# Kernel optimization log

Measured on AMD Instinct MI355X. Metric: run time of the kernel, lower is better.

## Reference

```python
import jax, jax.numpy as jnp
import numpy as np

B, D, DEPTH, H, E, N, NC = 128, 192, 12, 3, 4, 65, 100
WIN_HALF = 3  # window_size=7 -> |i-j| <= 3


def _ln(x, g, b, eps=1e-5):
    m = x.mean(-1, keepdims=True)
    v = ((x - m) ** 2).mean(-1, keepdims=True)
    return (x - m) / jnp.sqrt(v + eps) * g + b


def _forward(x, conv_w, conv_b, pe_g, pe_b, cls_token, pos_embed,
             n1_g, n1_b, qkv_w, temp, proj_w, proj_b, n2_g, n2_b,
             gate_w, gate_b, e_w1, e_b1, e_w2, e_b2, attn_scale, mlp_scale,
             norm_g, norm_b, hc_w, hc_b, head_w, head_b):
    Bx = x.shape[0]
    # patch embed: conv with kernel==stride==4 is a blocked matmul
    p = x.reshape(Bx, 3, 8, 4, 8, 4).transpose(0, 2, 4, 1, 3, 5).reshape(Bx, 64, 48)
    t = p @ conv_w.reshape(D, 48).T + conv_b
    t = _ln(t, pe_g, pe_b)
    t = jnp.concatenate([jnp.broadcast_to(cls_token, (Bx, 1, D)), t], axis=1) + pos_embed
    Nn = t.shape[1]
    hd = D // H
    scale = hd ** -0.5
    idx = jnp.arange(Nn)
    # local-window attention mask (log of {0,1} -> {-inf,0})
    mask = jnp.where(jnp.abs(idx[:, None] - idx[None, :]) <= WIN_HALF, 0.0, -jnp.inf)
    for l in range(DEPTH):
        # --- attention ---
        y = _ln(t, n1_g[l], n1_b[l])
        qkv = (y @ qkv_w[l].T).reshape(Bx, Nn, 3, H, hd).transpose(2, 0, 3, 1, 4)
        q, k, v = qkv[0], qkv[1], qkv[2]
        a = (q @ k.transpose(0, 1, 3, 2)) * scale / temp[l]  # [B,H,N,N]
        a = jax.nn.softmax(a + mask, axis=-1)
        o = (a @ v).transpose(0, 2, 1, 3).reshape(Bx, Nn, D)
        o = o @ proj_w[l].T + proj_b[l]
        t = t + attn_scale[l] * o
        # --- top-2 MoE (dense-equivalent of the masked per-expert dispatch) ---
        y = _ln(t, n2_g[l], n2_b[l])
        g = jax.nn.softmax(y @ gate_w[l].T + gate_b[l], axis=-1)  # [B,N,E]
        tg, ti = jax.lax.top_k(g, 2)
        tg = tg / tg.sum(-1, keepdims=True)
        h = jax.nn.gelu(jnp.einsum('bnc,ehc->bneh', y, e_w1[l]) + e_b1[l], approximate=False)
        eo = jnp.einsum('bneh,ech->bnec', h, e_w2[l]) + e_b2[l]  # [B,N,E,C]
        sel = jnp.take_along_axis(eo, ti[..., None], axis=2)  # [B,N,2,C]
        mo = (sel * tg[..., None]).sum(axis=2)
        t = t + mlp_scale[l] * mo
    t = _ln(t, norm_g, norm_b)
    cls = t[:, 0]
    # hypercomplex linear head: out[:,k] += x[:,j] @ W[(k-j)%n].T
    xv = cls.reshape(Bx, E, D // E)
    perm = (jnp.arange(E)[:, None] - jnp.arange(E)[None, :]) % E  # [k,j] -> i
    hh = jnp.einsum('bjc,kjoc->bko', xv, hc_w[perm]).reshape(Bx, 2 * D) + hc_b
    hh = jax.nn.gelu(hh, approximate=False)
    return hh @ head_w.T + head_b


def setup_inputs() -> dict:
    ks = iter(jax.random.split(jax.random.key(0), 64))
    def rn(shape, s=0.02):
        return jax.random.normal(next(ks), shape, jnp.float32) * s
    return dict(
        x=jax.random.normal(next(ks), (B, 3, 32, 32), jnp.float32),
        conv_w=rn((D, 3, 4, 4)), conv_b=jnp.zeros((D,)),
        pe_g=jnp.ones((D,)), pe_b=jnp.zeros((D,)),
        cls_token=rn((1, 1, D)), pos_embed=rn((1, N, D)),
        n1_g=jnp.ones((DEPTH, D)), n1_b=jnp.zeros((DEPTH, D)),
        qkv_w=rn((DEPTH, 3 * D, D)), temp=jnp.ones((DEPTH, H, 1, 1)),
        proj_w=rn((DEPTH, D, D)), proj_b=jnp.zeros((DEPTH, D)),
        n2_g=jnp.ones((DEPTH, D)), n2_b=jnp.zeros((DEPTH, D)),
        gate_w=rn((DEPTH, E, D)), gate_b=jnp.zeros((DEPTH, E)),
        e_w1=rn((DEPTH, E, 2 * D, D)), e_b1=jnp.zeros((DEPTH, E, 2 * D)),
        e_w2=rn((DEPTH, E, D, 2 * D)), e_b2=jnp.zeros((DEPTH, E, D)),
        attn_scale=jnp.ones((DEPTH,)), mlp_scale=jnp.ones((DEPTH,)),
        norm_g=jnp.ones((D,)), norm_b=jnp.zeros((D,)),
        hc_w=rn((E, 2 * D // E, D // E)), hc_b=jnp.zeros((2 * D,)),
        head_w=rn((NC, 2 * D)), head_b=jnp.zeros((NC,)),
    )


def reference(x, conv_w, conv_b, pe_g, pe_b, cls_token, pos_embed,
              n1_g, n1_b, qkv_w, temp, proj_w, proj_b, n2_g, n2_b,
              gate_w, gate_b, e_w1, e_b1, e_w2, e_b2, attn_scale, mlp_scale,
              norm_g, norm_b, hc_w, hc_b, head_w, head_b):
    return _forward(x, conv_w, conv_b, pe_g, pe_b, cls_token, pos_embed,
                    n1_g, n1_b, qkv_w, temp, proj_w, proj_b, n2_g, n2_b,
                    gate_w, gate_b, e_w1, e_b1, e_w2, e_b2, attn_scale, mlp_scale,
                    norm_g, norm_b, hc_w, hc_b, head_w, head_b)
```

## Files before the change

### kernel.cpp

```cpp
#include <hip/hip_runtime.h>
#include <cmath>

#define ROWS 8320
#define DD   192

typedef __attribute__((ext_vector_type(8))) _Float16 half8;
typedef __attribute__((ext_vector_type(4))) float floatx4;

#define GLD16(gp, lp) __builtin_amdgcn_global_load_lds( \
    (const __attribute__((address_space(1))) void*)(gp), \
    (__attribute__((address_space(3))) void*)(lp), 16, 0, 0)

#define MFMA_F16 __builtin_amdgcn_mfma_f32_16x16x32_f16

__device__ __forceinline__ float gelu_f(float x) {
    return 0.5f * x * (1.0f + erff(x * 0.70710678118654752440f));
}

__device__ __forceinline__ float blk_sum_192(float v, float* sbuf) {
    int tid = threadIdx.x;
    sbuf[tid] = v;
    __syncthreads();
    for (int off = 96; off >= 3; off >>= 1) {
        if (tid < off) sbuf[tid] += sbuf[tid + off];
        __syncthreads();
    }
    float r = sbuf[0] + sbuf[1] + sbuf[2];
    __syncthreads();
    return r;
}

__global__ __launch_bounds__(256) void cvt_h_kernel(
    const float* __restrict__ s, _Float16* __restrict__ d, long n8)
{
    long i = (long)blockIdx.x * 256 + threadIdx.x;
    if (i >= n8) return;
    const float* sp = s + i * 8;
    _Float16* dp = d + i * 8;
    #pragma unroll
    for (int j = 0; j < 8; j++) dp[j] = (_Float16)sp[j];
}

__global__ __launch_bounds__(256) void permw2h_kernel(
    const float* __restrict__ s, _Float16* __restrict__ d)
{
    long i = (long)blockIdx.x * 256 + threadIdx.x;
    if (i >= (long)12 * 192 * 192) return;
    int l = (int)(i / (192 * 192));
    int rem = (int)(i % (192 * 192));
    int n = rem / 192, p = rem % 192;
    int c0 = p * 8;
    int e = c0 / 384, k0 = c0 % 384;
    const float* sp = s + (((size_t)l * 4 + e) * 192 + n) * 384 + k0;
    _Float16* dp = d + i * 8;
    #pragma unroll
    for (int j = 0; j < 8; j++) dp[j] = (_Float16)sp[j];
}

__global__ __launch_bounds__(192) void embed_kernel(
    const float* __restrict__ x, const float* __restrict__ conv_w,
    const float* __restrict__ conv_b, const float* __restrict__ pe_g,
    const float* __restrict__ pe_b, const float* __restrict__ cls_tok,
    const float* __restrict__ pos, float* __restrict__ t)
{
    __shared__ float patch[48];
    __shared__ float red[192];
    int blk = blockIdx.x;
    int b = blk / 65, n = blk % 65;
    int tid = threadIdx.x;
    if (n == 0) {
        t[(size_t)b * 65 * DD + tid] = cls_tok[tid] + pos[tid];
        return;
    }
    int p = n - 1, gy = p / 8, gx = p % 8;
    if (tid < 48) {
        int c = tid / 16, iy = (tid % 16) / 4, ix = tid % 4;
        patch[tid] = x[((size_t)b * 3 + c) * 1024 + (size_t)(gy * 4 + iy) * 32 + (gx * 4 + ix)];
    }
    __syncthreads();
    float s = conv_b[tid];
    const float* w = conv_w + (size_t)tid * 48;
    #pragma unroll
    for (int f = 0; f < 48; f++) s += patch[f] * w[f];
    float mean = blk_sum_192(s, red) * (1.0f / 192.0f);
    float d = s - mean;
    float var = blk_sum_192(d * d, red) * (1.0f / 192.0f);
    float o = d * rsqrtf(var + 1e-5f) * pe_g[tid] + pe_b[tid];
    t[((size_t)b * 65 + n) * DD + tid] = o + pos[(size_t)n * DD + tid];
}

__global__ __launch_bounds__(256) void ln_kernel(
    const float* __restrict__ in, const float* __restrict__ ctb,
    float* __restrict__ tout,
    float* __restrict__ yf, _Float16* __restrict__ yh,
    const float* __restrict__ g, const float* __restrict__ bb, long in_stride, int nrows,
    const float* __restrict__ gwm, const float* __restrict__ gb,
    int4* __restrict__ gwout)
{
    int wave = threadIdx.x >> 6, lane = threadIdx.x & 63;
    int r = blockIdx.x * 4 + wave;
    if (r >= nrows) return;
    const float* row = in + (size_t)r * in_stride;
    float v0 = row[lane], v1 = row[lane + 64], v2 = row[lane + 128];
    if (ctb) {
        long gr = (long)r * (in_stride / DD);
        const float* cb = ctb + gr * 384;
        v0 += cb[lane] + cb[192 + lane];
        v1 += cb[lane + 64] + cb[256 + lane];
        v2 += cb[lane + 128] + cb[320 + lane];
        if (tout) {
            float* tr = tout + (size_t)r * in_stride;
            tr[lane] = v0; tr[lane + 64] = v1; tr[lane + 128] = v2;
        }
    }
    float s = v0 + v1 + v2;
    #pragma unroll
    for (int off = 32; off > 0; off >>= 1) s += __shfl_xor(s, off);
    float mean = s * (1.0f / 192.0f);
    float d0 = v0 - mean, d1 = v1 - mean, d2 = v2 - mean;
    float q = d0 * d0 + d1 * d1 + d2 * d2;
    #pragma unroll
    for (int off = 32; off > 0; off >>= 1) q += __shfl_xor(q, off);
    float rstd = rsqrtf(q * (1.0f / 192.0f) + 1e-5f);
    float o0 = d0 * rstd * g[lane] + bb[lane];
    float o1 = d1 * rstd * g[lane + 64] + bb[lane + 64];
    float o2 = d2 * rstd * g[lane + 128] + bb[lane + 128];
    if (yf) {
        float* yr = yf + (size_t)r * DD;
        yr[lane] = o0; yr[lane + 64] = o1; yr[lane + 128] = o2;
    }
    if (yh) {
        _Float16* yr = yh + (size_t)r * DD;
        yr[lane] = (_Float16)o0; yr[lane + 64] = (_Float16)o1; yr[lane + 128] = (_Float16)o2;
    }
    if (gwm) {
        float pe[4];
        #pragma unroll
        for (int e = 0; e < 4; e++) {
            const float* w = gwm + (size_t)e * DD;
            pe[e] = o0 * w[lane] + o1 * w[lane + 64] + o2 * w[lane + 128];
            #pragma unroll
            for (int off = 32; off > 0; off >>= 1) pe[e] += __shfl_xor(pe[e], off);
        }
        if (lane == 0) {
            #pragma unroll
            for (int e = 0; e < 4; e++) pe[e] += gb[e];
            float mx = fmaxf(fmaxf(pe[0], pe[1]), fmaxf(pe[2], pe[3]));
            float ex[4];
            #pragma unroll
            for (int e = 0; e < 4; e++) ex[e] = expf(pe[e] - mx);
            int i0 = 0;
            #pragma unroll
            for (int e = 1; e < 4; e++) if (ex[e] > ex[i0]) i0 = e;
            int i1 = (i0 == 0) ? 1 : 0;
            #pragma unroll
            for (int e = 0; e < 4; e++) if (e != i0 && ex[e] > ex[i1]) i1 = e;
            float denom = ex[i0] + ex[i1];
            int4 o4;
            o4.x = i0; o4.y = i1;
            o4.z = __float_as_int(ex[i0] / denom);
            o4.w = __float_as_int(ex[i1] / denom);
            gwout[r] = o4;
        }
    }
}

__global__ __launch_bounds__(256) void gate_build_kernel(
    const int4* __restrict__ gwrow, int* __restrict__ cnt,
    int* __restrict__ list, float* __restrict__ wlist, int rows)
{
    int r = blockIdx.x * 256 + threadIdx.x;
    int lane = threadIdx.x & 63;
    bool active = r < rows;
    int4 gv = active ? gwrow[r] : int4{-1, -1, 0, 0};
    #pragma unroll
    for (int e = 0; e < 4; e++) {
        bool sel = active && (gv.x == e || gv.y == e);
        int rank = (gv.x == e) ? 0 : 1;
        float w = (gv.x == e) ? __int_as_float(gv.z) : __int_as_float(gv.w);
        unsigned long long mask = __ballot(sel);
        int cw = __popcll(mask);
        if (cw) {
            int leader = __ffsll((long long)mask) - 1;
            int base = 0;
            if (lane == leader) base = atomicAdd(&cnt[e], cw);
            base = __shfl(base, leader);
            if (sel) {
                int idx = base + __popcll(mask & ((1ULL << lane) - 1ULL));
                list[(size_t)e * ROWS + idx] = (r << 1) | rank;
                wlist[(size_t)e * ROWS + idx] = w;
            }
        }
    }
}

template <int MODE>
__global__ __launch_bounds__(256) void gemm_h(
    const _Float16* __restrict__ A, const _Float16* __restrict__ W,
    int Nn, _Float16* __restrict__ outH, float* __restrict__ t,
    const float* __restrict__ bias, const float* __restrict__ scale)
{
    __shared__ __align__(16) _Float16 As[64 * 192];
    __shared__ __align__(16) _Float16 Ws[64 * 192];
    const int tid = threadIdx.x;
    const int lane = tid & 63, wave = tid >> 6;
    const int m0 = blockIdx.x * 64, n0 = blockIdx.y * 64;
    const int wm = (wave & 1) * 32, wn = (wave >> 1) * 32;
    const int lr = lane & 15, quad = lane >> 4;

    #pragma unroll
    for (int i = 0; i < 6; i++) {
        int s = (wave * 6 + i) * 64 + lane;
        int rr = s / 24, c = s % 24;
        GLD16(A + (size_t)(m0 + rr) * 192 + (c ^ (rr & 7)) * 8,
              (char*)As + (size_t)(wave * 6 + i) * 1024);
        GLD16(W + (size_t)(n0 + rr) * 192 + (c ^ (rr & 7)) * 8,
              (char*)Ws + (size_t)(wave * 6 + i) * 1024);
    }
    __syncthreads();

    floatx4 zero = {0.f, 0.f, 0.f, 0.f};
    floatx4 acc[2][2];
    acc[0][0] = zero; acc[0][1] = zero; acc[1][0] = zero; acc[1][1] = zero;

    #pragma unroll
    for (int m = 0; m < 6; m++) {
        int ch = m * 4 + quad;
        half8 a[2], w[2];
        #pragma unroll
        for (int ti = 0; ti < 2; ti++) {
            int ar = wm + ti * 16 + lr;
            a[ti] = *(const half8*)(As + ((size_t)ar * 24 + (ch ^ (ar & 7))) * 8);
            int cr = wn + ti * 16 + lr;
            w[ti] = *(const half8*)(Ws + ((size_t)cr * 24 + (ch ^ (cr & 7))) * 8);
        }
        #pragma unroll
        for (int ti = 0; ti < 2; ti++)
            #pragma unroll
            for (int tj = 0; tj < 2; tj++)
                acc[ti][tj] = MFMA_F16(a[ti], w[tj], acc[ti][tj], 0, 0, 0);
    }

    float sc = (MODE == 2) ? scale[0] : 0.f;
    #pragma unroll
    for (int ti = 0; ti < 2; ti++)
        #pragma unroll
        for (int tj = 0; tj < 2; tj++)
            #pragma unroll
            for (int r = 0; r < 4; r++) {
                int grow = m0 + wm + ti * 16 + quad * 4 + r;
                int gcol = n0 + wn + tj * 16 + lr;
                float v = acc[ti][tj][r];
                if (MODE == 0) {
                    float vp = __shfl_xor(v, 1);
                    if ((lane & 1) == 0) {
                        union { _Float16 h[2]; unsigned u; } pk;
                        pk.h[0] = (_Float16)v;
                        pk.h[1] = (_Float16)vp;
                        *(unsigned*)(outH + (size_t)grow * Nn + (gcol & ~1)) = pk.u;
                    }
                } else {
                    t[(size_t)grow * DD + gcol] += sc * (v + bias[gcol]);
                }
            }
}

__global__ __launch_bounds__(256) void moe_kernel(
    const _Float16* __restrict__ yh, const _Float16* __restrict__ w1,
    const _Float16* __restrict__ w2, const float* __restrict__ b1,
    const float* __restrict__ b2, const float* __restrict__ scale,
    const int* __restrict__ cnt, const int* __restrict__ list,
    const float* __restrict__ wlist, float* __restrict__ ctb)
{
    __shared__ __align__(16) _Float16 As[32 * 192];
    __shared__ __align__(16) _Float16 W1s[64 * 192];
    __shared__ __align__(16) _Float16 W2s[192 * 64];
    __shared__ __align__(16) _Float16 Hs[32 * 64];
    __shared__ int   rl[32];
    __shared__ int   rk[32];
    __shared__ float wl[32];
    const int e  = blockIdx.y;
    const int cnte = cnt[e];
    const int r0 = blockIdx.x * 32;
    if (r0 >= cnte) return;
    const int tid = threadIdx.x;
    const int lane = tid & 63, wave = tid >> 6;
    const int lr = lane & 15, quad = lane >> 4;
    const int wr = (wave & 1) * 16;
    const int wc1 = (wave >> 1) * 16;
    const int wc2 = (wave >> 1) * 96;

    if (tid < 32) {
        int sl = r0 + tid;
        bool ok = sl < cnte;
        int v = ok ? list[(size_t)e * ROWS + sl] : 0;
        rl[tid] = ok ? (v >> 1) : 0;
        rk[tid] = ok ? (v & 1) : -1;
        wl[tid] = ok ? wlist[(size_t)e * ROWS + sl] : 0.f;
    }
    __syncthreads();

    #pragma unroll
    for (int i = 0; i < 3; i++) {
        int s = (wave * 3 + i) * 64 + lane;
        int rr = s / 24, c = s % 24;
        GLD16(yh + (size_t)rl[rr] * 192 + (c ^ (rr & 7)) * 8,
              (char*)As + (size_t)(wave * 3 + i) * 1024);
    }
    #pragma unroll
    for (int i = 0; i < 6; i++) {
        int s = (wave * 6 + i) * 64 + lane;
        int rr = s / 24, c = s % 24;
        GLD16(w1 + ((size_t)e * 384 + rr) * 192 + (c ^ (rr & 7)) * 8,
              (char*)W1s + (size_t)(wave * 6 + i) * 1024);
    }
    __syncthreads();

    floatx4 zero = {0.f, 0.f, 0.f, 0.f};
    floatx4 acc2[6];
    #pragma unroll
    for (int j = 0; j < 6; j++) acc2[j] = zero;

    for (int nc = 0; nc < 6; nc++) {
        int ncg = e * 6 + nc;
        #pragma unroll
        for (int i = 0; i < 6; i++) {
            int s = (wave * 6 + i) * 64 + lane;
            int n = s >> 3, c = s & 7;
            GLD16(w2 + (size_t)n * 1536 + (ncg * 8 + (c ^ (n & 7))) * 8,
                  (char*)W2s + (size_t)(wave * 6 + i) * 1024);
        }
        floatx4 acc1[2];
        acc1[0] = zero; acc1[1] = zero;
        #pragma unroll
        for (int m = 0; m < 6; m++) {
            int ar = wr + lr;
            int ch = m * 4 + quad;
            half8 a = *(const half8*)(As + ((size_t)ar * 24 + (ch ^ (ar & 7))) * 8);
            #pragma unroll
            for (int tc = 0; tc < 2; tc++) {
                int cr = wc1 + tc * 32 + lr;
                half8 w = *(const half8*)(W1s + ((size_t)cr * 24 + (ch ^ (cr & 7))) * 8);
                acc1[tc] = MFMA_F16(a, w, acc1[tc], 0, 0, 0);
            }
        }
        #pragma unroll
        for (int tc = 0; tc < 2; tc++)
            #pragma unroll
            for (int r = 0; r < 4; r++) {
                int hrow = wr + quad * 4 + r;
                int hcol = wc1 + tc * 32 + lr;
                float v = gelu_f(acc1[tc][r] + b1[64 * ncg + hcol]) * wl[hrow];
                float vp = __shfl_xor(v, 1);
                if ((lane & 1) == 0) {
                    union { _Float16 h[2]; unsigned u; } pk;
                    pk.h[0] = (_Float16)v;
                    pk.h[1] = (_Float16)vp;
                    int cl = (hcol >> 3) ^ (hrow & 7);
                    *(unsigned*)(Hs + ((size_t)hrow * 8 + cl) * 8 + (hcol & 7)) = pk.u;
                }
            }
        __syncthreads();
        if (nc < 5) {
            #pragma unroll
            for (int i = 0; i < 6; i++) {
                int s = (wave * 6 + i) * 64 + lane;
                int rr = s / 24, c = s % 24;
                GLD16(w1 + ((size_t)e * 384 + (nc + 1) * 64 + rr) * 192 + (c ^ (rr & 7)) * 8,
                      (char*)W1s + (size_t)(wave * 6 + i) * 1024);
            }
        }
        #pragma unroll
        for (int kk = 0; kk < 2; kk++) {
            int ar = wr + lr;
            int ch = kk * 4 + quad;
            half8 a = *(const half8*)(Hs + ((size_t)ar * 8 + (ch ^ (ar & 7))) * 8);
            #pragma unroll
            for (int tj = 0; tj < 6; tj++) {
                int cr = wc2 + tj * 16 + lr;
                half8 w = *(const half8*)(W2s + ((size_t)cr * 8 + (ch ^ (cr & 7))) * 8);
                acc2[tj] = MFMA_F16(a, w, acc2[tj], 0, 0, 0);
            }
        }
        __syncthreads();
    }

    float sc = scale[0];
    #pragma unroll
    for (int tj = 0; tj < 6; tj++) {
        int gcol = wc2 + tj * 16 + lr;
        #pragma unroll
        for (int r = 0; r < 4; r++) {
            int lrow = wr + quad * 4 + r;
            int rank = rk[lrow];
            if (rank >= 0) {
                float v = sc * (acc2[tj][r] + wl[lrow] * b2[e * 192 + gcol]);
                ctb[((size_t)rl[lrow] * 2 + rank) * 192 + gcol] = v;
            }
        }
    }
}

__global__ __launch_bounds__(256) void attn_kernel(
    const _Float16* __restrict__ qkv, const float* __restrict__ temp,
    _Float16* __restrict__ o)
{
    __shared__ float q[65][64], k[65][64], v[65][64];
    __shared__ float p[65][8];
    int bh = blockIdx.x;
    int b = bh / 3, h = bh % 3;
    int tid = threadIdx.x;
    float coef = 0.125f / temp[h];
    const _Float16* base = qkv + (size_t)b * 65 * 576 + h * 64;
    for (int idx = tid; idx < 65 * 64; idx += 256) {
        int i = idx >> 6, d = idx & 63;
        q[i][d] = (float)base[(size_t)i * 576 + d];
        k[i][d] = (float)base[(size_t)i * 576 + 192 + d];
        v[i][d] = (float)base[(size_t)i * 576 + 384 + d];
    }
    __syncthreads();
    if (tid < 65) {
        int i = tid;
        float sc[7];
        float mx = -1e30f;
        #pragma unroll
        for (int jo = 0; jo < 7; jo++) {
            int j = i - 3 + jo;
            if (j >= 0 && j < 65) {
                float s = 0.f;
                #pragma unroll
                for (int d = 0; d < 64; d++) s += q[i][d] * k[j][d];
                sc[jo] = s * coef;
                mx = fmaxf(mx, sc[jo]);
            } else sc[jo] = -1e30f;
        }
        float sum = 0.f;
        #pragma unroll
        for (int jo = 0; jo < 7; jo++) {
            float e = expf(sc[jo] - mx);
            p[i][jo] = e;
            sum += e;
        }
        float inv = 1.0f / sum;
        #pragma unroll
        for (int jo = 0; jo < 7; jo++) p[i][jo] *= inv;
    }
    __syncthreads();
    for (int idx = tid; idx < 65 * 64; idx += 256) {
        int i = idx >> 6, d = idx & 63;
        float s = 0.f;
        #pragma unroll
        for (int jo = 0; jo < 7; jo++) {
            int j = i - 3 + jo;
            if (j >= 0 && j < 65) s += p[i][jo] * v[j][d];
        }
        o[((size_t)b * 65 + i) * 192 + h * 64 + d] = (_Float16)s;
    }
}

__global__ __launch_bounds__(128) void head_kernel(
    const float* __restrict__ cls, const float* __restrict__ hc_w,
    const float* __restrict__ hc_b, const float* __restrict__ head_w,
    const float* __restrict__ head_b, float* __restrict__ out)
{
    __shared__ float c[192];
    __shared__ float hh[384];
    int b = blockIdx.x, tid = threadIdx.x;
    for (int i = tid; i < 192; i += 128) c[i] = cls[(size_t)b * 192 + i];
    __syncthreads();
    for (int i = tid; i < 384; i += 128) {
        int k = i / 96, o = i % 96;
        float s = hc_b[i];
        #pragma unroll
        for (int j = 0; j < 4; j++) {
            int pp = (k - j + 4) & 3;
            const float* w = hc_w + ((size_t)pp * 96 + o) * 48;
            const float* xv = c + j * 48;
            #pragma unroll
            for (int cc = 0; cc < 48; cc++) s += xv[cc] * w[cc];
        }
        hh[i] = gelu_f(s);
    }
    __syncthreads();
    for (int i = tid; i < 100; i += 128) {
        float s = head_b[i];
        const float* w = head_w + (size_t)i * 384;
        for (int kk = 0; kk < 384; kk++) s += hh[kk] * w[kk];
        out[(size_t)b * 100 + i] = s;
    }
}

extern "C" void kernel_launch(void* const* d_in, const int* in_sizes, int n_in,
                              void* d_out, int out_size, void* d_ws, size_t ws_size,
                              hipStream_t stream)
{
    const float* x        = (const float*)d_in[0];
    const float* conv_w   = (const float*)d_in[1];
    const float* conv_b   = (const float*)d_in[2];
    const float* pe_g     = (const float*)d_in[3];
    const float* pe_b     = (const float*)d_in[4];
    const float* cls_tok  = (const float*)d_in[5];
    const float* pos      = (const float*)d_in[6];
    const float* n1_g     = (const float*)d_in[7];
    const float* n1_b     = (const float*)d_in[8];
    const float* qkv_w    = (const float*)d_in[9];
    const float* temp     = (const float*)d_in[10];
    const float* proj_w   = (const float*)d_in[11];
    const float* proj_b   = (const float*)d_in[12];
    const float* n2_g     = (const float*)d_in[13];
    const float* n2_b     = (const float*)d_in[14];
    const float* gate_w   = (const float*)d_in[15];
    const float* gate_b   = (const float*)d_in[16];
    const float* e_w1     = (const float*)d_in[17];
    const float* e_b1     = (const float*)d_in[18];
    const float* e_w2     = (const float*)d_in[19];
    const float* e_b2     = (const float*)d_in[20];
    const float* attn_sc  = (const float*)d_in[21];
    const float* mlp_sc   = (const float*)d_in[22];
    const float* norm_g   = (const float*)d_in[23];
    const float* norm_b   = (const float*)d_in[24];
    const float* hc_w     = (const float*)d_in[25];
    const float* hc_b     = (const float*)d_in[26];
    const float* head_w   = (const float*)d_in[27];
    const float* head_b   = (const float*)d_in[28];

    char* base = (char*)d_ws;
    float*  t     = (float*)base;   base += (size_t)ROWS * DD * 4;
    float*  ctb   = (float*)base;   base += (size_t)ROWS * 384 * 4;
    int4*   gwrow = (int4*)base;    base += (size_t)ROWS * 16;
    int*    cnts  = (int*)base;     base += (size_t)12 * 4 * sizeof(int) + 64;
    int*    elist = (int*)base;     base += (size_t)4 * ROWS * 4;
    float*  ewls  = (float*)base;   base += (size_t)4 * ROWS * 4;
    float*  ycls  = (float*)base;   base += (size_t)128 * DD * 4;
    _Float16* yhb = (_Float16*)base; base += (size_t)ROWS * DD * 2;
    _Float16* qkvh = (_Float16*)base; base += (size_t)ROWS * 576 * 2;
    _Float16* osph = (_Float16*)base; base += (size_t)ROWS * DD * 2;
    _Float16* qkvw_h = (_Float16*)base; base += (size_t)12 * 576 * 192 * 2;
    _Float16* projw_h = (_Float16*)base; base += (size_t)12 * 192 * 192 * 2;
    _Float16* ew1_h = (_Float16*)base; base += (size_t)12 * 1536 * 192 * 2;
    _Float16* ew2_h = (_Float16*)base; base += (size_t)12 * 192 * 1536 * 2;

    hipMemsetAsync(cnts, 0, 12 * 4 * sizeof(int), stream);

    {
        long n8 = (long)12 * 576 * 192 / 8;
        cvt_h_kernel<<<(int)((n8 + 255) / 256), 256, 0, stream>>>(qkv_w, qkvw_h, n8);
        n8 = (long)12 * 192 * 192 / 8;
        cvt_h_kernel<<<(int)((n8 + 255) / 256), 256, 0, stream>>>(proj_w, projw_h, n8);
        n8 = (long)12 * 1536 * 192 / 8;
        cvt_h_kernel<<<(int)((n8 + 255) / 256), 256, 0, stream>>>(e_w1, ew1_h, n8);
        long n = (long)12 * 192 * 192;
        permw2h_kernel<<<(int)((n + 255) / 256), 256, 0, stream>>>(e_w2, ew2_h);
    }

    embed_kernel<<<128 * 65, 192, 0, stream>>>(x, conv_w, conv_b, pe_g, pe_b, cls_tok, pos, t);

    for (int l = 0; l < 12; l++) {
        ln_kernel<<<ROWS / 4, 256, 0, stream>>>(
            t, (l > 0) ? ctb : nullptr, (l > 0) ? t : nullptr,
            nullptr, yhb, n1_g + l * DD, n1_b + l * DD, DD, ROWS,
            nullptr, nullptr, nullptr);
        gemm_h<0><<<dim3(130, 9), 256, 0, stream>>>(
            yhb, qkvw_h + (size_t)l * 576 * 192, 576, qkvh, nullptr, nullptr, nullptr);
        attn_kernel<<<128 * 3, 256, 0, stream>>>(qkvh, temp + l * 3, osph);
        gemm_h<2><<<dim3(130, 3), 256, 0, stream>>>(
            osph, projw_h + (size_t)l * 192 * 192, 192, nullptr, t,
            proj_b + l * DD, attn_sc + l);
        ln_kernel<<<ROWS / 4, 256, 0, stream>>>(
            t, nullptr, nullptr, nullptr, yhb, n2_g + l * DD, n2_b + l * DD, DD, ROWS,
            gate_w + (size_t)l * 4 * DD, gate_b + l * 4, gwrow);
        gate_build_kernel<<<(ROWS + 255) / 256, 256, 0, stream>>>(
            gwrow, cnts + l * 4, elist, ewls, ROWS);
        moe_kernel<<<dim3(260, 4), 256, 0, stream>>>(
            yhb, ew1_h + (size_t)l * 1536 * 192, ew2_h + (size_t)l * 192 * 1536,
            e_b1 + (size_t)l * 1536, e_b2 + (size_t)l * 4 * 192, mlp_sc + l,
            cnts + l * 4, elist, ewls, ctb);
    }

    ln_kernel<<<32, 256, 0, stream>>>(
        t, ctb, nullptr, ycls, nullptr, norm_g, norm_b, (long)65 * DD, 128,
        nullptr, nullptr, nullptr);
    head_kernel<<<128, 128, 0, stream>>>(ycls, hc_w, hc_b, head_w, head_b, (float*)d_out);
}
```

Measured before the change: 1.341 ms.

## Software-pipeline MoE expert kernel with double-buffered 32-wide hidden chunks

Restructures the MoE kernel's hidden-dimension loop from 6 chunks of 64 to 12 chunks of 32, with double-buffered W1, W2 and H tiles in shared memory. The second GEMM for chunk n-1 now runs in the same iteration as the first GEMM for chunk n, so each iteration needs one barrier instead of two, and the W1 prefetch for the next chunk is issued earlier. The goal is to overlap global-to-LDS weight loads and cut synchronisation stalls. In exchange there are more loop iterations with less MFMA work each, and the W2 and H LDS swizzle changes to a 4-chunk pattern, which may cause bank conflicts.

```diff
diff --git a/kernel.cpp b/kernel.cpp
--- a/kernel.cpp
+++ b/kernel.cpp
@@ -273,9 +273,9 @@
     const float* __restrict__ wlist, float* __restrict__ ctb)
 {
     __shared__ __align__(16) _Float16 As[32 * 192];
-    __shared__ __align__(16) _Float16 W1s[64 * 192];
-    __shared__ __align__(16) _Float16 W2s[192 * 64];
-    __shared__ __align__(16) _Float16 Hs[32 * 64];
+    __shared__ __align__(16) _Float16 W1s[2][32 * 192];
+    __shared__ __align__(16) _Float16 W2s[2][192 * 32];
+    __shared__ __align__(16) _Float16 Hs[2][32 * 32];
     __shared__ int   rl[32];
     __shared__ int   rk[32];
     __shared__ float wl[32];
@@ -286,7 +286,7 @@
     const int tid = threadIdx.x;
     const int lane = tid & 63, wave = tid >> 6;
     const int lr = lane & 15, quad = lane >> 4;
-    const int wr = (wave & 1) * 16;
+    const int wr  = (wave & 1) * 16;
     const int wc1 = (wave >> 1) * 16;
     const int wc2 = (wave >> 1) * 96;
 
@@ -294,7 +294,7 @@
         int sl = r0 + tid;
         bool ok = sl < cnte;
         int v = ok ? list[(size_t)e * ROWS + sl] : 0;
-        rl[tid] = ok ? (v >> 1) : 0;
+        rl[tid] = v >> 1;
         rk[tid] = ok ? (v & 1) : -1;
         wl[tid] = ok ? wlist[(size_t)e * ROWS + sl] : 0.f;
     }
@@ -304,15 +304,14 @@
     for (int i = 0; i < 3; i++) {
         int s = (wave * 3 + i) * 64 + lane;
         int rr = s / 24, c = s % 24;
-        GLD16(yh + (size_t)rl[rr] * 192 + (c ^ (rr & 7)) * 8,
-              (char*)As + (size_t)(wave * 3 + i) * 1024);
-    }
-    #pragma unroll
-    for (int i = 0; i < 6; i++) {
-        int s = (wave * 6 + i) * 64 + lane;
+        GLD16(yh + (size_t)rl[rr] * 192 + (c ^ (rr & 7)) * 8, (char*)As + s * 16);
+    }
+    #pragma unroll
+    for (int i = 0; i < 3; i++) {
+        int s = (wave * 3 + i) * 64 + lane;
         int rr = s / 24, c = s % 24;
         GLD16(w1 + ((size_t)e * 384 + rr) * 192 + (c ^ (rr & 7)) * 8,
-              (char*)W1s + (size_t)(wave * 6 + i) * 1024);
+              (char*)W1s[0] + s * 16);
     }
     __syncthreads();
 
@@ -320,72 +319,75 @@
     floatx4 acc2[6];
     #pragma unroll
     for (int j = 0; j < 6; j++) acc2[j] = zero;
-
-    for (int nc = 0; nc < 6; nc++) {
-        int ncg = e * 6 + nc;
-        #pragma unroll
-        for (int i = 0; i < 6; i++) {
-            int s = (wave * 6 + i) * 64 + lane;
-            int n = s >> 3, c = s & 7;
-            GLD16(w2 + (size_t)n * 1536 + (ncg * 8 + (c ^ (n & 7))) * 8,
-                  (char*)W2s + (size_t)(wave * 6 + i) * 1024);
-        }
-        floatx4 acc1[2];
-        acc1[0] = zero; acc1[1] = zero;
+    const float sc = scale[0];
+
+    #pragma unroll
+    for (int nc = 0; nc < 12; nc++) {
+        const int p = nc & 1;
+        const int ncg = e * 12 + nc;
+        if (nc < 11) {
+            #pragma unroll
+            for (int i = 0; i < 3; i++) {
+                int s = (wave * 3 + i) * 64 + lane;
+                int rr = s / 24, c = s % 24;
+                GLD16(w1 + ((size_t)e * 384 + (nc + 1) * 32 + rr) * 192 + (c ^ (rr & 7)) * 8,
+                      (char*)W1s[1 - p] + s * 16);
+            }
+        }
+        #pragma unroll
+        for (int i = 0; i < 3; i++) {
+            int s = (wave * 3 + i) * 64 + lane;
+            int n = s >> 2, c = s & 3;
+            GLD16(w2 + (size_t)n * 1536 + ((size_t)ncg * 4 + (c ^ ((n >> 2) & 3))) * 8,
+                  (char*)W2s[p] + s * 16);
+        }
+        floatx4 acc1 = zero;
         #pragma unroll
         for (int m = 0; m < 6; m++) {
+            int ch = m * 4 + quad;
             int ar = wr + lr;
-            int ch = m * 4 + quad;
             half8 a = *(const half8*)(As + ((size_t)ar * 24 + (ch ^ (ar & 7))) * 8);
-            #pragma unroll
-            for (int tc = 0; tc < 2; tc++) {
-                int cr = wc1 + tc * 32 + lr;
-                half8 w = *(const half8*)(W1s + ((size_t)cr * 24 + (ch ^ (cr & 7))) * 8);
-                acc1[tc] = MFMA_F16(a, w, acc1[tc], 0, 0, 0);
+            int cr = wc1 + lr;
+            half8 w = *(const half8*)(W1s[p] + ((size_t)cr * 24 + (ch ^ (cr & 7))) * 8);
+            acc1 = MFMA_F16(a, w, acc1, 0, 0, 0);
+        }
+        #pragma unroll
+        for (int r = 0; r < 4; r++) {
+            int hrow = wr + quad * 4 + r;
+            int hcol = wc1 + lr;
+            float v = gelu_f(acc1[r] + b1[32 * ncg + hcol]) * wl[hrow];
+            float vp = __shfl_xor(v, 1);
+            if ((lane & 1) == 0) {
+                union { _Float16 h[2]; unsigned u; } pk;
+                pk.h[0] = (_Float16)v;
+                pk.h[1] = (_Float16)vp;
+                int cl = (hcol >> 3) ^ ((hrow >> 2) & 3);
+                *(unsigned*)(Hs[p] + ((size_t)hrow * 4 + cl) * 8 + (hcol & 6)) = pk.u;
             }
         }
-        #pragma unroll
-        for (int tc = 0; tc < 2; tc++)
-            #pragma unroll
-            for (int r = 0; r < 4; r++) {
-                int hrow = wr + quad * 4 + r;
-                int hcol = wc1 + tc * 32 + lr;
-                float v = gelu_f(acc1[tc][r] + b1[64 * ncg + hcol]) * wl[hrow];
-                float vp = __shfl_xor(v, 1);
-                if ((lane & 1) == 0) {
-                    union { _Float16 h[2]; unsigned u; } pk;
-                    pk.h[0] = (_Float16)v;
-                    pk.h[1] = (_Float16)vp;
-                    int cl = (hcol >> 3) ^ (hrow & 7);
-                    *(unsigned*)(Hs + ((size_t)hrow * 8 + cl) * 8 + (hcol & 7)) = pk.u;
-                }
-            }
-        __syncthreads();
-        if (nc < 5) {
-            #pragma unroll
-            for (int i = 0; i < 6; i++) {
-                int s = (wave * 6 + i) * 64 + lane;
-                int rr = s / 24, c = s % 24;
-                GLD16(w1 + ((size_t)e * 384 + (nc + 1) * 64 + rr) * 192 + (c ^ (rr & 7)) * 8,
-                      (char*)W1s + (size_t)(wave * 6 + i) * 1024);
-            }
-        }
-        #pragma unroll
-        for (int kk = 0; kk < 2; kk++) {
+        if (nc > 0) {
             int ar = wr + lr;
-            int ch = kk * 4 + quad;
-            half8 a = *(const half8*)(Hs + ((size_t)ar * 8 + (ch ^ (ar & 7))) * 8);
+            half8 a = *(const half8*)(Hs[1 - p] + ((size_t)ar * 4 + (quad ^ ((ar >> 2) & 3))) * 8);
             #pragma unroll
             for (int tj = 0; tj < 6; tj++) {
                 int cr = wc2 + tj * 16 + lr;
-                half8 w = *(const half8*)(W2s + ((size_t)cr * 8 + (ch ^ (cr & 7))) * 8);
+                half8 w = *(const half8*)(W2s[1 - p] + ((size_t)cr * 4 + (quad ^ ((cr >> 2) & 3))) * 8);
                 acc2[tj] = MFMA_F16(a, w, acc2[tj], 0, 0, 0);
             }
         }
         __syncthreads();
     }
-
-    float sc = scale[0];
+    {
+        int ar = wr + lr;
+        half8 a = *(const half8*)(Hs[1] + ((size_t)ar * 4 + (quad ^ ((ar >> 2) & 3))) * 8);
+        #pragma unroll
+        for (int tj = 0; tj < 6; tj++) {
+            int cr = wc2 + tj * 16 + lr;
+            half8 w = *(const half8*)(W2s[1] + ((size_t)cr * 4 + (quad ^ ((cr >> 2) & 3))) * 8);
+            acc2[tj] = MFMA_F16(a, w, acc2[tj], 0, 0, 0);
+        }
+    }
+
     #pragma unroll
     for (int tj = 0; tj < 6; tj++) {
         int gcol = wc2 + tj * 16 + lr;
```

Measured after the change: 1.367 ms. No clear change (+1.9%).

## Fuse LN1, QKV GEMM, window attention, proj, LN2 and gating into one per-batch kernel

Applied to the files above, without the earlier changes.

Replaces the per-layer chain of LN1, QKV GEMM, attention, projection GEMM, LN2 plus gating, and gate-list build with a single kernel. Each block handles half of one batch's 65 tokens (with a 3-token halo) and keeps qkv and the attention output in LDS, so the qkv and attention-output global intermediates are no longer written and read back. Residual t is ping-ponged between two buffers, and the MoE expert lists are now filled by per-row atomics instead of a separate ballot kernel. The trade-offs are only 256 blocks with large LDS use (low occupancy), redundant halo K/V/QKV computation, weight reloads per block, and more atomic contention.

```diff
diff --git a/kernel.cpp b/kernel.cpp
--- a/kernel.cpp
+++ b/kernel.cpp
@@ -91,11 +91,8 @@
 
 __global__ __launch_bounds__(256) void ln_kernel(
     const float* __restrict__ in, const float* __restrict__ ctb,
-    float* __restrict__ tout,
-    float* __restrict__ yf, _Float16* __restrict__ yh,
-    const float* __restrict__ g, const float* __restrict__ bb, long in_stride, int nrows,
-    const float* __restrict__ gwm, const float* __restrict__ gb,
-    int4* __restrict__ gwout)
+    float* __restrict__ yf,
+    const float* __restrict__ g, const float* __restrict__ bb, long in_stride, int nrows)
 {
     int wave = threadIdx.x >> 6, lane = threadIdx.x & 63;
     int r = blockIdx.x * 4 + wave;
@@ -108,10 +105,6 @@
         v0 += cb[lane] + cb[192 + lane];
         v1 += cb[lane + 64] + cb[256 + lane];
         v2 += cb[lane + 128] + cb[320 + lane];
-        if (tout) {
-            float* tr = tout + (size_t)r * in_stride;
-            tr[lane] = v0; tr[lane + 64] = v1; tr[lane + 128] = v2;
-        }
     }
     float s = v0 + v1 + v2;
     #pragma unroll
@@ -122,18 +115,221 @@
     #pragma unroll
     for (int off = 32; off > 0; off >>= 1) q += __shfl_xor(q, off);
     float rstd = rsqrtf(q * (1.0f / 192.0f) + 1e-5f);
-    float o0 = d0 * rstd * g[lane] + bb[lane];
-    float o1 = d1 * rstd * g[lane + 64] + bb[lane + 64];
-    float o2 = d2 * rstd * g[lane + 128] + bb[lane + 128];
-    if (yf) {
-        float* yr = yf + (size_t)r * DD;
-        yr[lane] = o0; yr[lane + 64] = o1; yr[lane + 128] = o2;
-    }
-    if (yh) {
-        _Float16* yr = yh + (size_t)r * DD;
+    float* yr = yf + (size_t)r * DD;
+    yr[lane] = d0 * rstd * g[lane] + bb[lane];
+    yr[lane + 64] = d1 * rstd * g[lane + 64] + bb[lane + 64];
+    yr[lane + 128] = d2 * rstd * g[lane + 128] + bb[lane + 128];
+}
+
+__global__ __launch_bounds__(256) void layer_attn_kernel(
+    const float* __restrict__ tA, float* __restrict__ tB,
+    const float* __restrict__ ctb,
+    const _Float16* __restrict__ qw, const _Float16* __restrict__ pw,
+    const float* __restrict__ pb, const float* __restrict__ asc,
+    const float* __restrict__ temp,
+    const float* __restrict__ n1g, const float* __restrict__ n1b,
+    const float* __restrict__ n2g, const float* __restrict__ n2b,
+    const float* __restrict__ gwm, const float* __restrict__ gb,
+    _Float16* __restrict__ yhb,
+    int* __restrict__ cnt, int* __restrict__ list, float* __restrict__ wlist)
+{
+    __shared__ __align__(16) _Float16 ylds[48 * 200];
+    __shared__ __align__(16) _Float16 qkvlds[48 * 584];
+    __shared__ __align__(16) _Float16 wlds[192 * 192];
+    __shared__ float plds[33 * 3 * 8];
+
+    const int tid = threadIdx.x;
+    const int lane = tid & 63, wave = tid >> 6;
+    const int lr = lane & 15, quad = lane >> 4;
+    const int b = blockIdx.x >> 1, s = blockIdx.x & 1;
+    const int qlo = s ? 33 : 0, nq = s ? 32 : 33;
+    const int klo = s ? 30 : 0, nk = s ? 35 : 36;
+    const int qoff = qlo - klo;
+
+    floatx4 zero = {0.f, 0.f, 0.f, 0.f};
+
+    #pragma unroll
+    for (int i = 0; i < 18; i++) {
+        int sl = i * 256 + tid;
+        int rr = sl / 24, c = sl % 24;
+        GLD16(qw + (size_t)rr * 192 + (c ^ (rr & 7)) * 8, (char*)wlds + sl * 16);
+    }
+
+    for (int rl = wave; rl < nk; rl += 4) {
+        int gr = b * 65 + klo + rl;
+        const float* row = tA + (size_t)gr * DD;
+        float v0 = row[lane], v1 = row[lane + 64], v2 = row[lane + 128];
+        if (ctb) {
+            const float* cb = ctb + (size_t)gr * 384;
+            v0 += cb[lane] + cb[192 + lane];
+            v1 += cb[lane + 64] + cb[256 + lane];
+            v2 += cb[lane + 128] + cb[320 + lane];
+        }
+        float sm = v0 + v1 + v2;
+        #pragma unroll
+        for (int off = 32; off > 0; off >>= 1) sm += __shfl_xor(sm, off);
+        float mean = sm * (1.0f / 192.0f);
+        float d0 = v0 - mean, d1 = v1 - mean, d2 = v2 - mean;
+        float q = d0 * d0 + d1 * d1 + d2 * d2;
+        #pragma unroll
+        for (int off = 32; off > 0; off >>= 1) q += __shfl_xor(q, off);
+        float rstd = rsqrtf(q * (1.0f / 192.0f) + 1e-5f);
+        ylds[rl * 200 + lane]       = (_Float16)(d0 * rstd * n1g[lane] + n1b[lane]);
+        ylds[rl * 200 + lane + 64]  = (_Float16)(d1 * rstd * n1g[lane + 64] + n1b[lane + 64]);
+        ylds[rl * 200 + lane + 128] = (_Float16)(d2 * rstd * n1g[lane + 128] + n1b[lane + 128]);
+    }
+    __syncthreads();
+
+    for (int cs = 0; cs < 3; cs++) {
+        if (cs > 0) {
+            __syncthreads();
+            #pragma unroll
+            for (int i = 0; i < 18; i++) {
+                int sl = i * 256 + tid;
+                int rr = sl / 24, c = sl % 24;
+                GLD16(qw + ((size_t)cs * 192 + rr) * 192 + (c ^ (rr & 7)) * 8,
+                      (char*)wlds + sl * 16);
+            }
+            __syncthreads();
+        }
+        #pragma unroll
+        for (int mi = 0; mi < 3; mi++) {
+            floatx4 acc[3];
+            acc[0] = zero; acc[1] = zero; acc[2] = zero;
+            #pragma unroll
+            for (int m = 0; m < 6; m++) {
+                int ar = mi * 16 + lr;
+                half8 a = *(const half8*)(ylds + ar * 200 + m * 32 + quad * 8);
+                #pragma unroll
+                for (int ni = 0; ni < 3; ni++) {
+                    int n = wave * 48 + ni * 16 + lr;
+                    half8 w = *(const half8*)(wlds + ((size_t)n * 24 + ((m * 4 + quad) ^ (n & 7))) * 8);
+                    acc[ni] = MFMA_F16(a, w, acc[ni], 0, 0, 0);
+                }
+            }
+            #pragma unroll
+            for (int ni = 0; ni < 3; ni++)
+                #pragma unroll
+                for (int r = 0; r < 4; r++) {
+                    int row = mi * 16 + quad * 4 + r;
+                    int ncol = cs * 192 + wave * 48 + ni * 16 + lr;
+                    float v = acc[ni][r];
+                    float vp = __shfl_xor(v, 1);
+                    if ((lane & 1) == 0) {
+                        union { _Float16 h[2]; unsigned u; } pk;
+                        pk.h[0] = (_Float16)v; pk.h[1] = (_Float16)vp;
+                        *(unsigned*)(qkvlds + (size_t)row * 584 + (ncol & ~1)) = pk.u;
+                    }
+                }
+        }
+    }
+    __syncthreads();
+
+    #pragma unroll
+    for (int i = 0; i < 18; i++) {
+        int sl = i * 256 + tid;
+        int rr = sl / 24, c = sl % 24;
+        GLD16(pw + (size_t)rr * 192 + (c ^ (rr & 7)) * 8, (char*)wlds + sl * 16);
+    }
+
+    if (tid < nq * 3) {
+        int iq = tid / 3, h = tid % 3;
+        int ti = qlo + iq;
+        float coef = 0.125f / temp[h];
+        const _Float16* qrow = qkvlds + (size_t)(qoff + iq) * 584 + h * 64;
+        float sc[7]; float mx = -1e30f;
+        #pragma unroll
+        for (int jo = 0; jo < 7; jo++) {
+            int tj = ti - 3 + jo;
+            if (tj >= 0 && tj < 65) {
+                const _Float16* krow = qkvlds + (size_t)(tj - klo) * 584 + 192 + h * 64;
+                float ss = 0.f;
+                #pragma unroll
+                for (int d = 0; d < 64; d++) ss += (float)qrow[d] * (float)krow[d];
+                sc[jo] = ss * coef; mx = fmaxf(mx, sc[jo]);
+            } else sc[jo] = -1e30f;
+        }
+        float sum = 0.f;
+        #pragma unroll
+        for (int jo = 0; jo < 7; jo++) {
+            float e = expf(sc[jo] - mx);
+            plds[(iq * 3 + h) * 8 + jo] = e;
+            sum += e;
+        }
+        float inv = 1.0f / sum;
+        #pragma unroll
+        for (int jo = 0; jo < 7; jo++) plds[(iq * 3 + h) * 8 + jo] *= inv;
+    }
+    __syncthreads();
+
+    for (int idx = tid; idx < nq * 192; idx += 256) {
+        int iq = idx / 192, c = idx % 192;
+        int h = c >> 6, d = c & 63;
+        int ti = qlo + iq;
+        float ss = 0.f;
+        #pragma unroll
+        for (int jo = 0; jo < 7; jo++) {
+            int tj = ti - 3 + jo;
+            if (tj >= 0 && tj < 65)
+                ss += plds[(iq * 3 + h) * 8 + jo]
+                    * (float)qkvlds[(size_t)(tj - klo) * 584 + 384 + h * 64 + d];
+        }
+        ylds[iq * 200 + c] = (_Float16)ss;
+    }
+    __syncthreads();
+
+    float* tn = (float*)qkvlds;
+    float sca = asc[0];
+    #pragma unroll
+    for (int mi = 0; mi < 3; mi++) {
+        floatx4 acc[3];
+        acc[0] = zero; acc[1] = zero; acc[2] = zero;
+        #pragma unroll
+        for (int m = 0; m < 6; m++) {
+            int ar = mi * 16 + lr;
+            half8 a = *(const half8*)(ylds + ar * 200 + m * 32 + quad * 8);
+            #pragma unroll
+            for (int ni = 0; ni < 3; ni++) {
+                int n = wave * 48 + ni * 16 + lr;
+                half8 w = *(const half8*)(wlds + ((size_t)n * 24 + ((m * 4 + quad) ^ (n & 7))) * 8);
+                acc[ni] = MFMA_F16(a, w, acc[ni], 0, 0, 0);
+            }
+        }
+        #pragma unroll
+        for (int ni = 0; ni < 3; ni++)
+            #pragma unroll
+            for (int r = 0; r < 4; r++) {
+                int row = mi * 16 + quad * 4 + r;
+                int n = wave * 48 + ni * 16 + lr;
+                if (row < nq) {
+                    int gr = b * 65 + qlo + row;
+                    float base = tA[(size_t)gr * DD + n];
+                    if (ctb) base += ctb[(size_t)gr * 384 + n] + ctb[(size_t)gr * 384 + 192 + n];
+                    float v = base + sca * (acc[ni][r] + pb[n]);
+                    tB[(size_t)gr * DD + n] = v;
+                    tn[row * 196 + n] = v;
+                }
+            }
+    }
+    __syncthreads();
+
+    for (int rl = wave; rl < nq; rl += 4) {
+        int gr = b * 65 + qlo + rl;
+        float v0 = tn[rl * 196 + lane], v1 = tn[rl * 196 + 64 + lane], v2 = tn[rl * 196 + 128 + lane];
+        float sm = v0 + v1 + v2;
+        #pragma unroll
+        for (int off = 32; off > 0; off >>= 1) sm += __shfl_xor(sm, off);
+        float mean = sm * (1.0f / 192.0f);
+        float d0 = v0 - mean, d1 = v1 - mean, d2 = v2 - mean;
+        float q = d0 * d0 + d1 * d1 + d2 * d2;
+        #pragma unroll
+        for (int off = 32; off > 0; off >>= 1) q += __shfl_xor(q, off);
+        float rstd = rsqrtf(q * (1.0f / 192.0f) + 1e-5f);
+        float o0 = d0 * rstd * n2g[lane] + n2b[lane];
+        float o1 = d1 * rstd * n2g[lane + 64] + n2b[lane + 64];
+        float o2 = d2 * rstd * n2g[lane + 128] + n2b[lane + 128];
+        _Float16* yr = yhb + (size_t)gr * DD;
         yr[lane] = (_Float16)o0; yr[lane + 64] = (_Float16)o1; yr[lane + 128] = (_Float16)o2;
-    }
-    if (gwm) {
         float pe[4];
         #pragma unroll
         for (int e = 0; e < 4; e++) {
@@ -156,113 +352,14 @@
             #pragma unroll
             for (int e = 0; e < 4; e++) if (e != i0 && ex[e] > ex[i1]) i1 = e;
             float denom = ex[i0] + ex[i1];
-            int4 o4;
-            o4.x = i0; o4.y = i1;
-            o4.z = __float_as_int(ex[i0] / denom);
-            o4.w = __float_as_int(ex[i1] / denom);
-            gwout[r] = o4;
-        }
-    }
-}
-
-__global__ __launch_bounds__(256) void gate_build_kernel(
-    const int4* __restrict__ gwrow, int* __restrict__ cnt,
-    int* __restrict__ list, float* __restrict__ wlist, int rows)
-{
-    int r = blockIdx.x * 256 + threadIdx.x;
-    int lane = threadIdx.x & 63;
-    bool active = r < rows;
-    int4 gv = active ? gwrow[r] : int4{-1, -1, 0, 0};
-    #pragma unroll
-    for (int e = 0; e < 4; e++) {
-        bool sel = active && (gv.x == e || gv.y == e);
-        int rank = (gv.x == e) ? 0 : 1;
-        float w = (gv.x == e) ? __int_as_float(gv.z) : __int_as_float(gv.w);
-        unsigned long long mask = __ballot(sel);
-        int cw = __popcll(mask);
-        if (cw) {
-            int leader = __ffsll((long long)mask) - 1;
-            int base = 0;
-            if (lane == leader) base = atomicAdd(&cnt[e], cw);
-            base = __shfl(base, leader);
-            if (sel) {
-                int idx = base + __popcll(mask & ((1ULL << lane) - 1ULL));
-                list[(size_t)e * ROWS + idx] = (r << 1) | rank;
-                wlist[(size_t)e * ROWS + idx] = w;
-            }
-        }
-    }
-}
-
-template <int MODE>
-__global__ __launch_bounds__(256) void gemm_h(
-    const _Float16* __restrict__ A, const _Float16* __restrict__ W,
-    int Nn, _Float16* __restrict__ outH, float* __restrict__ t,
-    const float* __restrict__ bias, const float* __restrict__ scale)
-{
-    __shared__ __align__(16) _Float16 As[64 * 192];
-    __shared__ __align__(16) _Float16 Ws[64 * 192];
-    const int tid = threadIdx.x;
-    const int lane = tid & 63, wave = tid >> 6;
-    const int m0 = blockIdx.x * 64, n0 = blockIdx.y * 64;
-    const int wm = (wave & 1) * 32, wn = (wave >> 1) * 32;
-    const int lr = lane & 15, quad = lane >> 4;
-
-    #pragma unroll
-    for (int i = 0; i < 6; i++) {
-        int s = (wave * 6 + i) * 64 + lane;
-        int rr = s / 24, c = s % 24;
-        GLD16(A + (size_t)(m0 + rr) * 192 + (c ^ (rr & 7)) * 8,
-              (char*)As + (size_t)(wave * 6 + i) * 1024);
-        GLD16(W + (size_t)(n0 + rr) * 192 + (c ^ (rr & 7)) * 8,
-              (char*)Ws + (size_t)(wave * 6 + i) * 1024);
-    }
-    __syncthreads();
-
-    floatx4 zero = {0.f, 0.f, 0.f, 0.f};
-    floatx4 acc[2][2];
-    acc[0][0] = zero; acc[0][1] = zero; acc[1][0] = zero; acc[1][1] = zero;
-
-    #pragma unroll
-    for (int m = 0; m < 6; m++) {
-        int ch = m * 4 + quad;
-        half8 a[2], w[2];
-        #pragma unroll
-        for (int ti = 0; ti < 2; ti++) {
-            int ar = wm + ti * 16 + lr;
-            a[ti] = *(const half8*)(As + ((size_t)ar * 24 + (ch ^ (ar & 7))) * 8);
-            int cr = wn + ti * 16 + lr;
-            w[ti] = *(const half8*)(Ws + ((size_t)cr * 24 + (ch ^ (cr & 7))) * 8);
-        }
-        #pragma unroll
-        for (int ti = 0; ti < 2; ti++)
-            #pragma unroll
-            for (int tj = 0; tj < 2; tj++)
-                acc[ti][tj] = MFMA_F16(a[ti], w[tj], acc[ti][tj], 0, 0, 0);
-    }
-
-    float sc = (MODE == 2) ? scale[0] : 0.f;
-    #pragma unroll
-    for (int ti = 0; ti < 2; ti++)
-        #pragma unroll
-        for (int tj = 0; tj < 2; tj++)
-            #pragma unroll
-            for (int r = 0; r < 4; r++) {
-                int grow = m0 + wm + ti * 16 + quad * 4 + r;
-                int gcol = n0 + wn + tj * 16 + lr;
-                float v = acc[ti][tj][r];
-                if (MODE == 0) {
-                    float vp = __shfl_xor(v, 1);
-                    if ((lane & 1) == 0) {
-                        union { _Float16 h[2]; unsigned u; } pk;
-                        pk.h[0] = (_Float16)v;
-                        pk.h[1] = (_Float16)vp;
-                        *(unsigned*)(outH + (size_t)grow * Nn + (gcol & ~1)) = pk.u;
-                    }
-                } else {
-                    t[(size_t)grow * DD + gcol] += sc * (v + bias[gcol]);
-                }
-            }
+            int idx0 = atomicAdd(&cnt[i0], 1);
+            list[(size_t)i0 * ROWS + idx0] = (gr << 1) | 0;
+            wlist[(size_t)i0 * ROWS + idx0] = ex[i0] / denom;
+            int idx1 = atomicAdd(&cnt[i1], 1);
+            list[(size_t)i1 * ROWS + idx1] = (gr << 1) | 1;
+            wlist[(size_t)i1 * ROWS + idx1] = ex[i1] / denom;
+        }
+    }
 }
 
 __global__ __launch_bounds__(256) void moe_kernel(
@@ -294,7 +391,7 @@
         int sl = r0 + tid;
         bool ok = sl < cnte;
         int v = ok ? list[(size_t)e * ROWS + sl] : 0;
-        rl[tid] = ok ? (v >> 1) : 0;
+        rl[tid] = v >> 1;
         rk[tid] = ok ? (v & 1) : -1;
         wl[tid] = ok ? wlist[(size_t)e * ROWS + sl] : 0.f;
     }
@@ -398,63 +495,6 @@
                 ctb[((size_t)rl[lrow] * 2 + rank) * 192 + gcol] = v;
             }
         }
-    }
-}
-
-__global__ __launch_bounds__(256) void attn_kernel(
-    const _Float16* __restrict__ qkv, const float* __restrict__ temp,
-    _Float16* __restrict__ o)
-{
-    __shared__ float q[65][64], k[65][64], v[65][64];
-    __shared__ float p[65][8];
-    int bh = blockIdx.x;
-    int b = bh / 3, h = bh % 3;
-    int tid = threadIdx.x;
-    float coef = 0.125f / temp[h];
-    const _Float16* base = qkv + (size_t)b * 65 * 576 + h * 64;
-    for (int idx = tid; idx < 65 * 64; idx += 256) {
-        int i = idx >> 6, d = idx & 63;
-        q[i][d] = (float)base[(size_t)i * 576 + d];
-        k[i][d] = (float)base[(size_t)i * 576 + 192 + d];
-        v[i][d] = (float)base[(size_t)i * 576 + 384 + d];
-    }
-    __syncthreads();
-    if (tid < 65) {
-        int i = tid;
-        float sc[7];
-        float mx = -1e30f;
-        #pragma unroll
-        for (int jo = 0; jo < 7; jo++) {
-            int j = i - 3 + jo;
-            if (j >= 0 && j < 65) {
-                float s = 0.f;
-                #pragma unroll
-                for (int d = 0; d < 64; d++) s += q[i][d] * k[j][d];
-                sc[jo] = s * coef;
-                mx = fmaxf(mx, sc[jo]);
-            } else sc[jo] = -1e30f;
-        }
-        float sum = 0.f;
-        #pragma unroll
-        for (int jo = 0; jo < 7; jo++) {
-            float e = expf(sc[jo] - mx);
-            p[i][jo] = e;
-            sum += e;
-        }
-        float inv = 1.0f / sum;
-        #pragma unroll
-        for (int jo = 0; jo < 7; jo++) p[i][jo] *= inv;
-    }
-    __syncthreads();
-    for (int idx = tid; idx < 65 * 64; idx += 256) {
-        int i = idx >> 6, d = idx & 63;
-        float s = 0.f;
-        #pragma unroll
-        for (int jo = 0; jo < 7; jo++) {
-            int j = i - 3 + jo;
-            if (j >= 0 && j < 65) s += p[i][jo] * v[j][d];
-        }
-        o[((size_t)b * 65 + i) * 192 + h * 64 + d] = (_Float16)s;
     }
 }
 
@@ -525,16 +565,14 @@
     const float* head_b   = (const float*)d_in[28];
 
     char* base = (char*)d_ws;
-    float*  t     = (float*)base;   base += (size_t)ROWS * DD * 4;
+    float*  t0    = (float*)base;   base += (size_t)ROWS * DD * 4;
+    float*  t1    = (float*)base;   base += (size_t)ROWS * DD * 4;
     float*  ctb   = (float*)base;   base += (size_t)ROWS * 384 * 4;
-    int4*   gwrow = (int4*)base;    base += (size_t)ROWS * 16;
     int*    cnts  = (int*)base;     base += (size_t)12 * 4 * sizeof(int) + 64;
     int*    elist = (int*)base;     base += (size_t)4 * ROWS * 4;
     float*  ewls  = (float*)base;   base += (size_t)4 * ROWS * 4;
     float*  ycls  = (float*)base;   base += (size_t)128 * DD * 4;
     _Float16* yhb = (_Float16*)base; base += (size_t)ROWS * DD * 2;
-    _Float16* qkvh = (_Float16*)base; base += (size_t)ROWS * 576 * 2;
-    _Float16* osph = (_Float16*)base; base += (size_t)ROWS * DD * 2;
     _Float16* qkvw_h = (_Float16*)base; base += (size_t)12 * 576 * 192 * 2;
     _Float16* projw_h = (_Float16*)base; base += (size_t)12 * 192 * 192 * 2;
     _Float16* ew1_h = (_Float16*)base; base += (size_t)12 * 1536 * 192 * 2;
@@ -553,24 +591,19 @@
         permw2h_kernel<<<(int)((n + 255) / 256), 256, 0, stream>>>(e_w2, ew2_h);
     }
 
-    embed_kernel<<<128 * 65, 192, 0, stream>>>(x, conv_w, conv_b, pe_g, pe_b, cls_tok, pos, t);
-
+    embed_kernel<<<128 * 65, 192, 0, stream>>>(x, conv_w, conv_b, pe_g, pe_b, cls_tok, pos, t0);
+
+    float* tbuf[2] = {t0, t1};
     for (int l = 0; l < 12; l++) {
-        ln_kernel<<<ROWS / 4, 256, 0, stream>>>(
-            t, (l > 0) ? ctb : nullptr, (l > 0) ? t : nullptr,
-            nullptr, yhb, n1_g + l * DD, n1_b + l * DD, DD, ROWS,
-            nullptr, nullptr, nullptr);
-        gemm_h<0><<<dim3(130, 9), 256, 0, stream>>>(
-            yhb, qkvw_h + (size_t)l * 576 * 192, 576, qkvh, nullptr, nullptr, nullptr);
-        attn_kernel<<<128 * 3, 256, 0, stream>>>(qkvh, temp + l * 3, osph);
-        gemm_h<2><<<dim3(130, 3), 256, 0, stream>>>(
-            osph, projw_h + (size_t)l * 192 * 192, 192, nullptr, t,
-            proj_b + l * DD, attn_sc + l);
-        ln_kernel<<<ROWS / 4, 256, 0, stream>>>(
-            t, nullptr, nullptr, nullptr, yhb, n2_g + l * DD, n2_b + l * DD, DD, ROWS,
-            gate_w + (size_t)l * 4 * DD, gate_b + l * 4, gwrow);
-        gate_build_kernel<<<(ROWS + 255) / 256, 256, 0, stream>>>(
-            gwrow, cnts + l * 4, elist, ewls, ROWS);
+        const float* tin = tbuf[l & 1];
+        float* tout = tbuf[1 - (l & 1)];
+        layer_attn_kernel<<<256, 256, 0, stream>>>(
+            tin, tout, (l > 0) ? ctb : nullptr,
+            qkvw_h + (size_t)l * 576 * 192, projw_h + (size_t)l * 192 * 192,
+            proj_b + l * DD, attn_sc + l, temp + l * 3,
+            n1_g + l * DD, n1_b + l * DD, n2_g + l * DD, n2_b + l * DD,
+            gate_w + (size_t)l * 4 * DD, gate_b + l * 4,
+            yhb, cnts + l * 4, elist, ewls);
         moe_kernel<<<dim3(260, 4), 256, 0, stream>>>(
             yhb, ew1_h + (size_t)l * 1536 * 192, ew2_h + (size_t)l * 192 * 1536,
             e_b1 + (size_t)l * 1536, e_b2 + (size_t)l * 4 * 192, mlp_sc + l,
@@ -578,7 +611,6 @@
     }
 
     ln_kernel<<<32, 256, 0, stream>>>(
-        t, ctb, nullptr, ycls, nullptr, norm_g, norm_b, (long)65 * DD, 128,
-        nullptr, nullptr, nullptr);
+        tbuf[0], ctb, ycls, norm_g, norm_b, (long)65 * DD, 128);
     head_kernel<<<128, 128, 0, stream>>>(ycls, hc_w, hc_b, head_w, head_b, (float*)d_out);
 }
```

After: 3.450 ms. 157% more time.
